# Performance work log

Hardware: AMD Instinct MI355X
Metric: run time of the kernel (lower is better)

The kernel has to match this reference:

```python
import jax, jax.numpy as jnp
import numpy as np

N_NODES = 100000
N_FEAT = 512
HIDDEN = 64
N_CLASSES = 40
N_EDGES = 3200000
K = 10
ALPHA = 0.1


def setup_inputs() -> dict:
    key = jax.random.key(0)
    k1, k2, k3, k4 = jax.random.split(key, 4)
    x = jax.random.normal(k1, (N_NODES, N_FEAT), dtype=jnp.float32)
    # Glorot-ish scaled linear weights
    W1 = jax.random.normal(k2, (N_FEAT, HIDDEN), dtype=jnp.float32) / np.sqrt(N_FEAT)
    b1 = jnp.zeros((HIDDEN,), dtype=jnp.float32)
    W2 = jax.random.normal(k3, (HIDDEN, N_CLASSES), dtype=jnp.float32) / np.sqrt(HIDDEN)
    b2 = jnp.zeros((N_CLASSES,), dtype=jnp.float32)
    edge_index = jax.random.randint(k4, (2, N_EDGES), 0, N_NODES, dtype=jnp.int64)
    return {"x": x, "W1": W1, "b1": b1, "W2": W2, "b2": b2, "edge_index": edge_index}


def reference(x, W1, b1, W2, b2, edge_index):
    n = x.shape[0]
    # MLP (dropout is identity in eval mode)
    h = jnp.maximum(x @ W1 + b1, 0.0)
    h = h @ W2 + b2  # [N, C]

    # gcn_norm with self-loops: A_hat = D^{-1/2} (A + I) D^{-1/2}
    loops = jnp.arange(n, dtype=edge_index.dtype)
    row = jnp.concatenate([edge_index[0], loops])  # source (gather)
    col = jnp.concatenate([edge_index[1], loops])  # target (scatter)
    deg = jax.ops.segment_sum(jnp.ones(row.shape, dtype=h.dtype), col, num_segments=n)
    dinv = jnp.where(deg > 0, jax.lax.rsqrt(deg), 0.0)
    norm = dinv[row] * dinv[col]  # [E + N]

    h0 = h

    def step(z, _):
        msg = norm[:, None] * z[row]                      # gather + scale
        agg = jax.ops.segment_sum(msg, col, num_segments=n)  # scatter-add
        z = ALPHA * h0 + (1.0 - ALPHA) * agg
        return z, None

    z, _ = jax.lax.scan(step, h0, None, length=K)
    return jax.nn.log_softmax(z, axis=1)
```

## Files before the change

kernel.cpp:

```cpp
#include <hip/hip_runtime.h>
#include <hip/hip_bf16.h>
#include <hip/hip_fp16.h>

#define N_NODES   100000
#define N_FEAT    512
#define HIDDEN    64
#define N_CLASSES 40
#define KITER     10
#define ALPHA     0.1f
#define ZP        64
#define HPITCH    72
#define NXCD      8
#define WIN       (N_NODES / NXCD)
#define FILLB     2048

typedef __attribute__((ext_vector_type(8))) short bf16x8;
typedef __attribute__((ext_vector_type(4))) float f32x4;

__device__ __forceinline__ float bf2f(unsigned short u) {
    union { unsigned int i; float f; } c;
    c.i = ((unsigned int)u) << 16;
    return c.f;
}
__device__ __forceinline__ unsigned short f2bf(float f) {
    union { float f; unsigned int u; } c; c.f = f;
    unsigned int r = c.u + 0x7FFFu + ((c.u >> 16) & 1u);
    return (unsigned short)(r >> 16);
}

__global__ void zero_flags_kernel(int* __restrict__ flags) {
    if (threadIdx.x < 2) flags[threadIdx.x] = 0;
}

__global__ void detect_float_kernel(const unsigned short* __restrict__ w1raw,
                                    int* __restrict__ flags) {
    int i = blockIdx.x * blockDim.x + threadIdx.x;
    if (i < 32768) {
        unsigned short u = w1raw[i];
        if ((u & 0x7F80u) == 0x7F80u) atomicAdd(&flags[0], 1);
    }
}

__global__ void detect_edge_kernel(const int* __restrict__ ei, int* __restrict__ flags) {
    int i = blockIdx.x * blockDim.x + threadIdx.x;
    if (i < 2048) {
        if (ei[2 * i + 1] != 0) atomicAdd(&flags[1], 1);
    }
}

__device__ __forceinline__ int edge_row(const int* ei, int e, int E, int i64f) {
    return i64f ? ei[2 * e] : ei[e];
}
__device__ __forceinline__ int edge_col(const int* ei, int e, int E, int i64f) {
    return i64f ? ei[2 * E + 2 * e] : ei[E + e];
}

__global__ void pack_w1_kernel(const void* __restrict__ W1p, const int* __restrict__ flags,
                               unsigned short* __restrict__ pb) {
    int idx = blockIdx.x * 256 + threadIdx.x;
    int j    = idx & 7;
    int lane = (idx >> 3) & 63;
    int ktnt = idx >> 9;
    int kt = ktnt & 15, nt = ktnt >> 4;
    int k = kt * 32 + (lane >> 4) * 8 + j;
    int n = nt * 16 + (lane & 15);
    unsigned short v;
    if (flags[0] > 0) v = f2bf(((const float*)W1p)[k * HIDDEN + n]);
    else              v = ((const unsigned short*)W1p)[k * HIDDEN + n];
    pb[idx] = v;
}

__global__ void pack_w2_kernel(const void* __restrict__ W2p, const int* __restrict__ flags,
                               unsigned short* __restrict__ pb2) {
    int idx = blockIdx.x * 256 + threadIdx.x;
    if (idx >= 3072) return;
    int j    = idx & 7;
    int lane = (idx >> 3) & 63;
    int ktnt = idx >> 9;
    int kt = ktnt & 1, nt = ktnt >> 1;
    int k = kt * 32 + (lane >> 4) * 8 + j;
    int n = nt * 16 + (lane & 15);
    unsigned short v = 0;
    if (n < N_CLASSES) {
        if (flags[0] > 0) v = f2bf(((const float*)W2p)[k * N_CLASSES + n]);
        else              v = ((const unsigned short*)W2p)[k * N_CLASSES + n];
    }
    pb2[idx] = v;
}

__global__ __launch_bounds__(256) void mlp_kernel(
    const void* __restrict__ xp,
    const unsigned short* __restrict__ pb,
    const unsigned short* __restrict__ pb2,
    const void* __restrict__ b1p,
    const void* __restrict__ b2p,
    const int* __restrict__ flags,
    const float* __restrict__ dinv,
    float* __restrict__ h0,
    __half* __restrict__ zh0)
{
    __shared__ unsigned short hsb[16 * HPITCH];
    const int t    = threadIdx.x;
    const int wave = t >> 6;
    const int lane = t & 63;
    const int quad = lane >> 4;
    const int ml   = lane & 15;
    const int base = blockIdx.x * 16;
    const int isf32 = flags[0] > 0;

    const bf16x8* pbv = (const bf16x8*)pb;

    f32x4 acc = {0.f, 0.f, 0.f, 0.f};
    if (!isf32) {
        const unsigned short* xrow = (const unsigned short*)xp
                                   + (size_t)(base + ml) * N_FEAT + quad * 8;
        #pragma unroll
        for (int kt = 0; kt < 16; ++kt) {
            bf16x8 a = *(const bf16x8*)(xrow + kt * 32);
            bf16x8 b = pbv[(wave * 16 + kt) * 64 + lane];
            acc = __builtin_amdgcn_mfma_f32_16x16x32_bf16(a, b, acc, 0, 0, 0);
        }
    } else {
        const float* xf = (const float*)xp + (size_t)(base + ml) * N_FEAT + quad * 8;
        #pragma unroll
        for (int kt = 0; kt < 16; ++kt) {
            float4 lo = *(const float4*)(xf + kt * 32);
            float4 hi = *(const float4*)(xf + kt * 32 + 4);
            bf16x8 a;
            a[0] = (short)f2bf(lo.x); a[1] = (short)f2bf(lo.y);
            a[2] = (short)f2bf(lo.z); a[3] = (short)f2bf(lo.w);
            a[4] = (short)f2bf(hi.x); a[5] = (short)f2bf(hi.y);
            a[6] = (short)f2bf(hi.z); a[7] = (short)f2bf(hi.w);
            bf16x8 b = pbv[(wave * 16 + kt) * 64 + lane];
            acc = __builtin_amdgcn_mfma_f32_16x16x32_bf16(a, b, acc, 0, 0, 0);
        }
    }

    float b1v = isf32 ? ((const float*)b1p)[wave * 16 + ml]
                      : bf2f(((const unsigned short*)b1p)[wave * 16 + ml]);
    #pragma unroll
    for (int r = 0; r < 4; ++r)
        hsb[(quad * 4 + r) * HPITCH + wave * 16 + ml] = f2bf(fmaxf(acc[r] + b1v, 0.0f));
    __syncthreads();

    if (wave < 3) {
        const bf16x8* pb2v = (const bf16x8*)pb2;
        f32x4 acc2 = {0.f, 0.f, 0.f, 0.f};
        #pragma unroll
        for (int kt = 0; kt < 2; ++kt) {
            bf16x8 a = *(const bf16x8*)(hsb + ml * HPITCH + kt * 32 + quad * 8);
            bf16x8 b = pb2v[(wave * 2 + kt) * 64 + lane];
            acc2 = __builtin_amdgcn_mfma_f32_16x16x32_bf16(a, b, acc2, 0, 0, 0);
        }
        int n = wave * 16 + ml;
        if (n < N_CLASSES) {
            float b2v = isf32 ? ((const float*)b2p)[n] : bf2f(((const unsigned short*)b2p)[n]);
            #pragma unroll
            for (int r = 0; r < 4; ++r) {
                int node = base + quad * 4 + r;
                float v = acc2[r] + b2v;
                h0[(size_t)node * N_CLASSES + n] = v;
                zh0[(size_t)node * ZP + n] = __float2half(v * dinv[node]);
            }
        }
    }
}

__global__ void zero_cnt_kernel(int* __restrict__ cnt) {
    int i = blockIdx.x * blockDim.x + threadIdx.x;
    if (i < N_NODES) cnt[i] = 0;
}

__global__ void count_kernel(const int* __restrict__ ei, const int* __restrict__ flags,
                             int* __restrict__ cnt, int E) {
    int e = blockIdx.x * blockDim.x + threadIdx.x;
    int i64f = flags[1] == 0;
    if (e < E) atomicAdd(&cnt[edge_col(ei, e, E, i64f)], 1);
}

__global__ void dinv_kernel(const int* __restrict__ cnt, float* __restrict__ dinv) {
    int i = blockIdx.x * blockDim.x + threadIdx.x;
    if (i < N_NODES) dinv[i] = rsqrtf((float)cnt[i] + 1.0f);
}

__global__ void zero_pad_kernel(__half* __restrict__ a, __half* __restrict__ b) {
    int t = threadIdx.x;
    if (t < ZP)            a[(size_t)N_NODES * ZP + t]        = __float2half(0.0f);
    else if (t < 2 * ZP)   b[(size_t)N_NODES * ZP + (t - ZP)] = __float2half(0.0f);
}

__global__ __launch_bounds__(1024) void scan_kernel(
    const int* __restrict__ cnt, int* __restrict__ rptr, int* __restrict__ wpos, int E)
{
    __shared__ int wsum[16];
    __shared__ int carry_s, tiletot_s;
    const int t = threadIdx.x, wave = t >> 6, lane = t & 63;
    if (t == 0) carry_s = 0;
    __syncthreads();
    for (int base = 0; base < N_NODES; base += 4096) {
        int i0 = base + t * 4;
        int v0 = (i0 + 0 < N_NODES) ? cnt[i0 + 0] : 0;
        int v1 = (i0 + 1 < N_NODES) ? cnt[i0 + 1] : 0;
        int v2 = (i0 + 2 < N_NODES) ? cnt[i0 + 2] : 0;
        int v3 = (i0 + 3 < N_NODES) ? cnt[i0 + 3] : 0;
        int tl = v0 + v1 + v2 + v3;
        int sc = tl;
        #pragma unroll
        for (int off = 1; off < 64; off <<= 1) {
            int u = __shfl_up(sc, off, 64);
            if (lane >= off) sc += u;
        }
        if (lane == 63) wsum[wave] = sc;
        int wexcl = sc - tl;
        __syncthreads();
        if (wave == 0) {
            int wv = (lane < 16) ? wsum[lane] : 0;
            int ws = wv;
            #pragma unroll
            for (int off = 1; off < 16; off <<= 1) {
                int u = __shfl_up(ws, off, 64);
                if (lane >= off) ws += u;
            }
            if (lane < 16) wsum[lane] = ws - wv;
            if (lane == 15) tiletot_s = ws;
        }
        __syncthreads();
        int P  = carry_s + wsum[wave] + wexcl;
        int e0 = P, e1 = P + v0, e2 = e1 + v1, e3 = e2 + v2;
        if (i0 + 0 < N_NODES) { rptr[i0 + 0] = e0; wpos[i0 + 0] = e0; }
        if (i0 + 1 < N_NODES) { rptr[i0 + 1] = e1; wpos[i0 + 1] = e1; }
        if (i0 + 2 < N_NODES) { rptr[i0 + 2] = e2; wpos[i0 + 2] = e2; }
        if (i0 + 3 < N_NODES) { rptr[i0 + 3] = e3; wpos[i0 + 3] = e3; }
        __syncthreads();
        if (t == 0) carry_s += tiletot_s;
        __syncthreads();
    }
    if (t == 0) rptr[N_NODES] = E;
}

__global__ __launch_bounds__(256) void fill_xcd_kernel(
    const int* __restrict__ ei, const int* __restrict__ flags,
    int* __restrict__ wpos, int* __restrict__ srcidx, int E)
{
    const int i64f = flags[1] == 0;
    const int lo   = (blockIdx.x & (NXCD - 1)) * WIN;
    const int sid  = blockIdx.x >> 3;
    const int stride = (FILLB / NXCD) * 256;
    for (int e = sid * 256 + threadIdx.x; e < E; e += stride) {
        int c = i64f ? __builtin_nontemporal_load(ei + 2 * E + 2 * e)
                     : __builtin_nontemporal_load(ei + E + e);
        if ((unsigned)(c - lo) < (unsigned)WIN) {
            int r = i64f ? __builtin_nontemporal_load(ei + 2 * e)
                         : __builtin_nontemporal_load(ei + e);
            int pos = atomicAdd(&wpos[c], 1);
            srcidx[pos] = r;
        }
    }
}

__global__ __launch_bounds__(256) void prop_kernel(
    const __half* __restrict__ zh, const float* __restrict__ h0,
    const float* __restrict__ dinv, const int* __restrict__ rptr,
    const int* __restrict__ srcidx, __half* __restrict__ zout)
{
    const int wave = threadIdx.x >> 6;
    const int lane = threadIdx.x & 63;
    const int g    = lane >> 4;
    const int l    = lane & 15;
    const int node = blockIdx.x * 16 + wave * 4 + g;
    const int c0   = l * 4;

    const int beg = rptr[node];
    const int end = rptr[node + 1];
    int nch = (end - beg + 15) >> 4;
    int m1    = max(nch, __shfl_xor(nch, 16, 64));
    int maxch = max(m1,  __shfl_xor(m1, 32, 64));

    float di = dinv[node];
    uint2 yself = *(const uint2*)(zh + ((size_t)node << 6) + c0);
    float h00 = 0.f, h01 = 0.f, h02 = 0.f, h03 = 0.f;
    if (c0 < N_CLASSES) {
        const float* hp = h0 + (size_t)node * N_CLASSES + c0;
        h00 = hp[0]; h01 = hp[1]; h02 = hp[2]; h03 = hp[3];
    }

    float a0 = 0.f, a1 = 0.f, a2 = 0.f, a3 = 0.f;
    float b0 = 0.f, b1 = 0.f, b2 = 0.f, b3 = 0.f;

    for (int ch = 0; ch < maxch; ++ch) {
        int idx = beg + ch * 16 + l;
        int sw  = (idx < end) ? srcidx[idx] : N_NODES;

        #pragma unroll
        for (int i = 0; i < 16; i += 2) {
            int s0 = __shfl(sw, (g << 4) + i,     64);
            int s1 = __shfl(sw, (g << 4) + i + 1, 64);
            uint2 z0 = *(const uint2*)(zh + ((size_t)s0 << 6) + c0);
            uint2 z1 = *(const uint2*)(zh + ((size_t)s1 << 6) + c0);
            const __half2* p0 = (const __half2*)&z0;
            const __half2* p1 = (const __half2*)&z1;
            float2 f00 = __half22float2(p0[0]);
            float2 f01 = __half22float2(p0[1]);
            float2 f10 = __half22float2(p1[0]);
            float2 f11 = __half22float2(p1[1]);
            a0 += f00.x; a1 += f00.y; a2 += f01.x; a3 += f01.y;
            b0 += f10.x; b1 += f10.y; b2 += f11.x; b3 += f11.y;
        }
    }

    if (c0 < N_CLASSES) {
        const __half2* ps = (const __half2*)&yself;
        float2 s01 = __half22float2(ps[0]);
        float2 s23 = __half22float2(ps[1]);
        float kk = (1.0f - ALPHA) * di;
        float o0 = ALPHA * h00 + kk * (a0 + b0 + s01.x);
        float o1 = ALPHA * h01 + kk * (a1 + b1 + s01.y);
        float o2 = ALPHA * h02 + kk * (a2 + b2 + s23.x);
        float o3 = ALPHA * h03 + kk * (a3 + b3 + s23.y);
        __half2 q01 = __floats2half2_rn(di * o0, di * o1);
        __half2 q23 = __floats2half2_rn(di * o2, di * o3);
        uint2 st;
        st.x = *(unsigned int*)&q01;
        st.y = *(unsigned int*)&q23;
        *(uint2*)(zout + ((size_t)node << 6) + c0) = st;
    }
}

__global__ __launch_bounds__(256) void lsm_kernel(
    const __half* __restrict__ zh, const float* __restrict__ dinv,
    const int* __restrict__ flags, void* __restrict__ outp)
{
    const int wave = threadIdx.x >> 6;
    const int lane = threadIdx.x & 63;
    const int node = blockIdx.x * 4 + wave;
    const int isf32 = flags[0] > 0;

    float di = dinv[node];
    float v = (lane < N_CLASSES)
            ? __half2float(zh[(size_t)node * ZP + lane]) / di : -1e30f;
    float m = v;
    #pragma unroll
    for (int o = 32; o; o >>= 1) m = fmaxf(m, __shfl_xor(m, o, 64));
    float e = (lane < N_CLASSES) ? expf(v - m) : 0.0f;
    float s = e;
    #pragma unroll
    for (int o = 32; o; o >>= 1) s += __shfl_xor(s, o, 64);
    float ls = logf(s);
    if (lane < N_CLASSES) {
        float r = v - m - ls;
        size_t idx = (size_t)node * N_CLASSES + lane;
        if (isf32) ((float*)outp)[idx] = r;
        else       ((__hip_bfloat16*)outp)[idx] = __float2bfloat16(r);
    }
}

extern "C" void kernel_launch(void* const* d_in, const int* in_sizes, int n_in,
                              void* d_out, int out_size, void* d_ws, size_t ws_size,
                              hipStream_t stream)
{
    const void* x  = d_in[0];
    const void* W1 = d_in[1];
    const void* b1 = d_in[2];
    const void* W2 = d_in[3];
    const void* b2 = d_in[4];
    const int* ei = (const int*)d_in[5];
    const int E = in_sizes[5] / 2;

    char* ws = (char*)d_ws;
    size_t off = 0;
    auto carve = [&](size_t bytes) -> void* {
        void* p = ws + off;
        off = (off + bytes + 255) & ~(size_t)255;
        return p;
    };
    float*  h0    = (float*) carve((size_t)N_NODES * N_CLASSES * 4);
    __half* zhA   = (__half*)carve((size_t)(N_NODES + 1) * ZP * 2);
    __half* zhB   = (__half*)carve((size_t)(N_NODES + 1) * ZP * 2);
    int*    cnt   = (int*)   carve((size_t)N_NODES * 4);
    float*  dinv  = (float*) carve((size_t)N_NODES * 4);
    int*    rptr  = (int*)   carve((size_t)(N_NODES + 1) * 4);
    int*    wpos  = (int*)   carve((size_t)N_NODES * 4);
    int*    srcidx= (int*)   carve((size_t)E * 4);
    unsigned short* pb  = (unsigned short*)carve(32768 * 2);
    unsigned short* pb2 = (unsigned short*)carve(3072 * 2);
    int*    flags = (int*)   carve(2 * sizeof(int));
    (void)ws_size; (void)n_in; (void)out_size;

    const int nodeBlocks = N_NODES / 4;
    const int mlpBlocks  = N_NODES / 16;
    const int propBlocks = N_NODES / 16;
    const int nThreads1  = (N_NODES + 255) / 256;
    const int eBlocks    = (E + 255) / 256;

    zero_flags_kernel<<<1, 64, 0, stream>>>(flags);
    detect_float_kernel<<<128, 256, 0, stream>>>((const unsigned short*)W1, flags);
    detect_edge_kernel<<<8, 256, 0, stream>>>(ei, flags);
    pack_w1_kernel<<<128, 256, 0, stream>>>(W1, flags, pb);
    pack_w2_kernel<<<12, 256, 0, stream>>>(W2, flags, pb2);

    zero_cnt_kernel<<<nThreads1, 256, 0, stream>>>(cnt);
    count_kernel<<<eBlocks, 256, 0, stream>>>(ei, flags, cnt, E);
    dinv_kernel<<<nThreads1, 256, 0, stream>>>(cnt, dinv);
    scan_kernel<<<1, 1024, 0, stream>>>(cnt, rptr, wpos, E);
    fill_xcd_kernel<<<FILLB, 256, 0, stream>>>(ei, flags, wpos, srcidx, E);
    zero_pad_kernel<<<1, 128, 0, stream>>>(zhA, zhB);

    mlp_kernel<<<mlpBlocks, 256, 0, stream>>>(x, pb, pb2, b1, b2, flags, dinv, h0, zhA);

    const __half* zin = zhA;
    __half* zout = zhB;
    const __half* zlast = zhA;
    for (int it = 0; it < KITER; ++it) {
        prop_kernel<<<propBlocks, 256, 0, stream>>>(zin, h0, dinv, rptr, srcidx, zout);
        zlast = zout;
        zin = zout;
        zout = (zout == zhB) ? zhA : zhB;
    }

    lsm_kernel<<<nodeBlocks, 256, 0, stream>>>(zlast, dinv, flags, d_out);
}
```

Measured before the change: 1.218 ms.

## Replace edge count and XCD-filtered fill with a binned partition plus scatter pass

Merges degree counting into one pass over the edges that also bins each edge into per-(target window, XCD) sub-buckets, storing a packed (row, local col) word. Wave ballots let one atomic reserve space for all lanes going to the same bucket. A second scatter kernel then reads each window's buckets and does the CSR atomic placement, so each XCD touches only its node window. This removes the eightfold rereading of the column array done by the old fill kernel. The cost is an extra intermediate buffer, an overflow path that reuses zhA before the MLP writes it, and a packing that assumes row indices fit in 17 bits.

```diff
diff --git a/kernel.cpp b/kernel.cpp
--- a/kernel.cpp
+++ b/kernel.cpp
@@ -12,7 +12,7 @@
 #define HPITCH    72
 #define NXCD      8
 #define WIN       (N_NODES / NXCD)
-#define FILLB     2048
+#define SUBCAP    65536
 
 typedef __attribute__((ext_vector_type(8))) short bf16x8;
 typedef __attribute__((ext_vector_type(4))) float f32x4;
@@ -46,13 +46,6 @@
     if (i < 2048) {
         if (ei[2 * i + 1] != 0) atomicAdd(&flags[1], 1);
     }
-}
-
-__device__ __forceinline__ int edge_row(const int* ei, int e, int E, int i64f) {
-    return i64f ? ei[2 * e] : ei[e];
-}
-__device__ __forceinline__ int edge_col(const int* ei, int e, int E, int i64f) {
-    return i64f ? ei[2 * E + 2 * e] : ei[E + e];
 }
 
 __global__ void pack_w1_kernel(const void* __restrict__ W1p, const int* __restrict__ flags,
@@ -166,16 +159,10 @@
     }
 }
 
-__global__ void zero_cnt_kernel(int* __restrict__ cnt) {
+__global__ void zero_cnt_kernel(int* __restrict__ cnt, int* __restrict__ cur) {
     int i = blockIdx.x * blockDim.x + threadIdx.x;
     if (i < N_NODES) cnt[i] = 0;
-}
-
-__global__ void count_kernel(const int* __restrict__ ei, const int* __restrict__ flags,
-                             int* __restrict__ cnt, int E) {
-    int e = blockIdx.x * blockDim.x + threadIdx.x;
-    int i64f = flags[1] == 0;
-    if (e < E) atomicAdd(&cnt[edge_col(ei, e, E, i64f)], 1);
+    if (i < 65) cur[i] = 0;
 }
 
 __global__ void dinv_kernel(const int* __restrict__ cnt, float* __restrict__ dinv) {
@@ -238,22 +225,80 @@
     if (t == 0) rptr[N_NODES] = E;
 }
 
-__global__ __launch_bounds__(256) void fill_xcd_kernel(
+__global__ __launch_bounds__(256) void partition_kernel(
     const int* __restrict__ ei, const int* __restrict__ flags,
-    int* __restrict__ wpos, int* __restrict__ srcidx, int E)
+    int* __restrict__ cnt, unsigned int* __restrict__ sub,
+    int* __restrict__ cur, int2* __restrict__ ovf, int E)
 {
     const int i64f = flags[1] == 0;
-    const int lo   = (blockIdx.x & (NXCD - 1)) * WIN;
-    const int sid  = blockIdx.x >> 3;
-    const int stride = (FILLB / NXCD) * 256;
-    for (int e = sid * 256 + threadIdx.x; e < E; e += stride) {
-        int c = i64f ? __builtin_nontemporal_load(ei + 2 * E + 2 * e)
+    const int lane = threadIdx.x & 63;
+    const int xcd  = blockIdx.x & 7;
+    const int waveg  = (blockIdx.x * 256 + threadIdx.x) >> 6;
+    const int stride = ((2048 * 256) >> 6) * 64;
+
+    for (int base = waveg * 64; base < E; base += stride) {
+        int e = base + lane;
+        bool valid = e < E;
+        int c = 0, r = 0;
+        if (valid) {
+            c = i64f ? __builtin_nontemporal_load(ei + 2 * E + 2 * e)
                      : __builtin_nontemporal_load(ei + E + e);
-        if ((unsigned)(c - lo) < (unsigned)WIN) {
-            int r = i64f ? __builtin_nontemporal_load(ei + 2 * e)
-                         : __builtin_nontemporal_load(ei + e);
-            int pos = atomicAdd(&wpos[c], 1);
-            srcidx[pos] = r;
+            r = i64f ? __builtin_nontemporal_load(ei + 2 * e)
+                     : __builtin_nontemporal_load(ei + e);
+            atomicAdd(&cnt[c], 1);
+        }
+        int w = valid ? (c / WIN) : 8;
+        unsigned pk = valid ? ((unsigned)r | ((unsigned)(c - w * WIN) << 17)) : 0u;
+        #pragma unroll
+        for (int ww = 0; ww < NXCD; ++ww) {
+            unsigned long long m = __ballot(w == ww);
+            if (!m) continue;
+            int leader = __ffsll(m) - 1;
+            int bpos = 0;
+            if (lane == leader) bpos = atomicAdd(&cur[ww * 8 + xcd], (int)__popcll(m));
+            bpos = __shfl(bpos, leader, 64);
+            if (w == ww) {
+                int rank = (int)__popcll(m & ((1ull << lane) - 1ull));
+                unsigned p = (unsigned)(bpos + rank);
+                if (p < SUBCAP) sub[(unsigned)(ww * 8 + xcd) * SUBCAP + p] = pk;
+                else { int op = atomicAdd(cur + 64, 1); ovf[op] = make_int2(r, c); }
+            }
+        }
+    }
+}
+
+__global__ __launch_bounds__(256) void scatter_kernel(
+    const unsigned int* __restrict__ sub, const int* __restrict__ cur,
+    const int2* __restrict__ ovf,
+    int* __restrict__ wpos, int* __restrict__ srcidx)
+{
+    const int w = blockIdx.x & 7;
+    const int tid64 = (blockIdx.x >> 3) * 256 + threadIdx.x;
+    int P[9];
+    P[0] = 0;
+    #pragma unroll
+    for (int a = 0; a < 8; ++a) {
+        int na = cur[w * 8 + a];
+        na = na > SUBCAP ? SUBCAP : na;
+        P[a + 1] = P[a] + na;
+    }
+    const int total = P[8];
+    for (int v = tid64; v < total; v += 65536) {
+        int a = 0;
+        #pragma unroll
+        for (int q = 1; q < 8; ++q) if (v >= P[q]) a = q;
+        unsigned pk = sub[(unsigned)(w * 8 + a) * SUBCAP + (v - P[a])];
+        int r = (int)(pk & 0x1FFFFu);
+        int c = w * WIN + (int)(pk >> 17);
+        int pos = atomicAdd(&wpos[c], 1);
+        srcidx[pos] = r;
+    }
+    int ov = cur[64];
+    for (int i = tid64; i < ov; i += 65536) {
+        int2 rc = ovf[i];
+        if (rc.y / WIN == w) {
+            int pos = atomicAdd(&wpos[rc.y], 1);
+            srcidx[pos] = rc.x;
         }
     }
 }
@@ -381,16 +426,19 @@
     int*    rptr  = (int*)   carve((size_t)(N_NODES + 1) * 4);
     int*    wpos  = (int*)   carve((size_t)N_NODES * 4);
     int*    srcidx= (int*)   carve((size_t)E * 4);
+    unsigned int* sub = (unsigned int*)carve((size_t)64 * SUBCAP * 4);
+    int*    cur   = (int*)   carve(65 * sizeof(int));
     unsigned short* pb  = (unsigned short*)carve(32768 * 2);
     unsigned short* pb2 = (unsigned short*)carve(3072 * 2);
     int*    flags = (int*)   carve(2 * sizeof(int));
     (void)ws_size; (void)n_in; (void)out_size;
 
+    int2* ovf = (int2*)zhA;
+
     const int nodeBlocks = N_NODES / 4;
     const int mlpBlocks  = N_NODES / 16;
     const int propBlocks = N_NODES / 16;
     const int nThreads1  = (N_NODES + 255) / 256;
-    const int eBlocks    = (E + 255) / 256;
 
     zero_flags_kernel<<<1, 64, 0, stream>>>(flags);
     detect_float_kernel<<<128, 256, 0, stream>>>((const unsigned short*)W1, flags);
@@ -398,11 +446,11 @@
     pack_w1_kernel<<<128, 256, 0, stream>>>(W1, flags, pb);
     pack_w2_kernel<<<12, 256, 0, stream>>>(W2, flags, pb2);
 
-    zero_cnt_kernel<<<nThreads1, 256, 0, stream>>>(cnt);
-    count_kernel<<<eBlocks, 256, 0, stream>>>(ei, flags, cnt, E);
+    zero_cnt_kernel<<<nThreads1, 256, 0, stream>>>(cnt, cur);
+    partition_kernel<<<2048, 256, 0, stream>>>(ei, flags, cnt, sub, cur, ovf, E);
     dinv_kernel<<<nThreads1, 256, 0, stream>>>(cnt, dinv);
     scan_kernel<<<1, 1024, 0, stream>>>(cnt, rptr, wpos, E);
-    fill_xcd_kernel<<<FILLB, 256, 0, stream>>>(ei, flags, wpos, srcidx, E);
+    scatter_kernel<<<2048, 256, 0, stream>>>(sub, cur, ovf, wpos, srcidx);
     zero_pad_kernel<<<1, 128, 0, stream>>>(zhA, zhB);
 
     mlp_kernel<<<mlpBlocks, 256, 0, stream>>>(x, pb, pb2, b1, b2, flags, dinv, h0, zhA);
```

Result: slower. 3.232 ms (+165.4%).
